# Kernel tuning notes

Measured on AMD Instinct MI355X. Metric: run time of the kernel, lower is better.

## Reference

```python
import jax, jax.numpy as jnp
import numpy as np

TOPK = 20
EPS = 1e-5
NEG_SLOPE = 0.2


def _bn(x, gamma, beta):
    # BatchNorm1d in training mode: stats over all but the channel (last) axis.
    axes = tuple(range(x.ndim - 1))
    m = x.mean(axes, keepdims=True)
    v = x.var(axes, keepdims=True)  # biased variance, as torch uses for normalization
    return (x - m) * jax.lax.rsqrt(v + EPS) * gamma + beta


def setup_inputs() -> dict:
    key = jax.random.key(0)
    ks = jax.random.split(key, 12)
    B, N, F, D, K = 64, 512, 64, 64, TOPK
    H = 32  # slide_win // 2
    return {
        "data": jax.random.normal(ks[0], (B, N, F), jnp.float32),
        "org_edge_index": jax.random.randint(ks[1], (2, 10), 0, N),  # unused by forward math
        "emb_table": jax.random.normal(ks[2], (N, D), jnp.float32) * 0.1,
        "W_gnn": jax.random.normal(ks[3], (D, F), jnp.float32) / jnp.sqrt(F),
        "att_i": jax.random.normal(ks[4], (D,), jnp.float32) / jnp.sqrt(D),
        "att_j": jax.random.normal(ks[5], (D,), jnp.float32) / jnp.sqrt(D),
        "att_em_i": jax.random.normal(ks[6], (D,), jnp.float32) / jnp.sqrt(D),
        "att_em_j": jax.random.normal(ks[7], (D,), jnp.float32) / jnp.sqrt(D),
        "bias_gnn": jnp.zeros((D,), jnp.float32),
        "bn1_g": jnp.ones((D,), jnp.float32), "bn1_b": jnp.zeros((D,), jnp.float32),
        "bn2_g": jnp.ones((D,), jnp.float32), "bn2_b": jnp.zeros((D,), jnp.float32),
        "lin_W": jax.random.normal(ks[8], (H, D), jnp.float32) / jnp.sqrt(D),
        "lin_b": jnp.zeros((H,), jnp.float32),
        "out_W": jax.random.normal(ks[9], (2 * H, H), jnp.float32) / jnp.sqrt(H),
        "out_b": jnp.zeros((2 * H,), jnp.float32),
    }


def reference(data, org_edge_index, emb_table, W_gnn, att_i, att_j, att_em_i, att_em_j,
              bias_gnn, bn1_g, bn1_b, bn2_g, bn2_b, lin_W, lin_b, out_W, out_b):
    B, N, F = data.shape
    # --- top-k cosine-similarity graph (embeddings are detached in the original) ---
    w = emb_table  # (N, D)
    nrm = jnp.linalg.norm(w, axis=-1)
    cos = (w @ w.T) / (nrm[:, None] * nrm[None, :])
    _, topk_idx = jax.lax.top_k(cos, TOPK)  # (N, K); col 0 is the self loop (cos=1)
    # Every target node i has exactly TOPK incoming edges j in topk_idx[i];
    # remove_self_loops + add_self_loops is set-equivalent to this edge set.

    # --- GraphLayer (GAT-style, heads=1, concat=False) ---
    xw = jnp.einsum('bnf,df->bnd', data, W_gnn)  # (B, N, D)
    a_i = xw @ att_i + w @ att_em_i              # (B, N), per-target scalar
    a_j = xw @ att_j + w @ att_em_j              # (B, N), per-source scalar
    alpha = a_i[:, :, None] + a_j[:, topk_idx]   # (B, N, K): gather sources per target
    alpha = jax.nn.leaky_relu(alpha, NEG_SLOPE)
    alpha = jax.nn.softmax(alpha, axis=-1)       # segment softmax over fixed-size neighborhoods
    xj = xw[:, topk_idx]                         # (B, N, K, D) edge gather (memory-bound)
    out = jnp.einsum('bnk,bnkd->bnd', alpha, xj) + bias_gnn  # scatter-aggregate

    # GNNLayer: BatchNorm1d over (B*N) rows + ReLU
    out = jax.nn.relu(_bn(out, bn1_g, bn1_b))

    # --- head ---
    out = out * w                                 # x * embedding(idx)
    out = jax.nn.relu(_bn(out, bn2_g, bn2_b))     # bn_outlayer_in over (B, D, N)
    out = out @ lin_W.T + lin_b                   # (B, N, slide_win//2)
    out = out @ out_W.T + out_b                   # OutLayer, single Linear -> (B, N, slide_win)
    return out
```

## Files before the change

### kernel.cpp

```cpp
#include <hip/hip_runtime.h>
#include <math.h>

#define Bb 64
#define Nn 512
#define Ff 64
#define Dd 64
#define Kk 20
#define Hh 32
#define ROWS (Bb*Nn)
#define EPSc 1e-5f
#define NEG 0.2f


__device__ __forceinline__ float dot4(float4 a, float4 b) {
    return a.x*b.x + a.y*b.y + a.z*b.z + a.w*b.w;
}
__device__ __forceinline__ void xr4(float4& a, int m) {
    a.x += __shfl_xor(a.x, m); a.y += __shfl_xor(a.y, m);
    a.z += __shfl_xor(a.z, m); a.w += __shfl_xor(a.w, m);
}

__global__ __launch_bounds__(256) void k_p1(const float* __restrict__ data,
                                            const float* __restrict__ emb,
                                            const float* __restrict__ Wg,
                                            const float* __restrict__ att_i,
                                            const float* __restrict__ att_j,
                                            const float* __restrict__ att_em_i,
                                            const float* __restrict__ att_em_j,
                                            int* __restrict__ topk,
                                            float* __restrict__ ai,
                                            float* __restrict__ aj,
                                            float* __restrict__ xw) {
    __shared__ __align__(16) float shbuf[576];
    int t = threadIdx.x, blk = blockIdx.x;
    if (blk < Nn) {
        float* wish = shbuf;
        float* sv   = shbuf + 64;
        int i = blk;
        if (t < 64) {
            float wv = emb[i*64 + t];
            float ss = wv*wv;
            #pragma unroll
            for (int s = 32; s > 0; s >>= 1) ss += __shfl_xor(ss, s);
            wish[t] = wv * (1.f / sqrtf(ss));
        }
        __syncthreads();
        int seg = t & 3, jl = t >> 2;
        const float4* wish4 = (const float4*)wish;
        float4 wn[4];
        #pragma unroll
        for (int q = 0; q < 4; q++) wn[q] = wish4[seg*4 + q];
        const float4* emb4 = (const float4*)emb;
        for (int jb = 0; jb < 8; jb++) {
            int j = jb*64 + jl;
            float p = 0.f, s2 = 0.f;
            #pragma unroll
            for (int q = 0; q < 4; q++) {
                float4 e = emb4[j*16 + seg*4 + q];
                p += dot4(e, wn[q]); s2 += dot4(e, e);
            }
            p  += __shfl_xor(p, 1);  p  += __shfl_xor(p, 2);
            s2 += __shfl_xor(s2, 1); s2 += __shfl_xor(s2, 2);
            if (seg == 0) sv[j] = p * (1.f / sqrtf(s2));
        }
        __syncthreads();
        if (t < 64) {
            float v[8];
            #pragma unroll
            for (int q = 0; q < 8; q++) v[q] = sv[q*64 + t];
            for (int k = 0; k < Kk; k++) {
                float bv = v[0]; int bi = t;
                #pragma unroll
                for (int q = 1; q < 8; q++)
                    if (v[q] > bv) { bv = v[q]; bi = q*64 + t; }
                #pragma unroll
                for (int s = 1; s < 64; s <<= 1) {
                    float ov = __shfl_xor(bv, s); int oi = __shfl_xor(bi, s);
                    if (ov > bv || (ov == bv && oi < bi)) { bv = ov; bi = oi; }
                }
                if (t == 0) topk[i*Kk + k] = bi;
                #pragma unroll
                for (int q = 0; q < 8; q++)
                    if (bi == q*64 + t) v[q] = -INFINITY;
            }
        }
    } else {
        float* sh = shbuf;
        int d = t & 63, r = t >> 6;
        const float4* wg4 = (const float4*)Wg;
        float4 w4[16];
        #pragma unroll
        for (int q = 0; q < 16; q++) w4[q] = wg4[d*16 + q];
        float atti = att_i[d], attj = att_j[d];
        float aemi = att_em_i[d], aemj = att_em_j[d];
        const float4* sh4 = (const float4*)sh;
        for (int it = 0; it < 16; it++) {
            int g = (blk - Nn)*16 + it;
            sh[t] = data[g*256 + t];
            float acc = 0.f;
            #pragma unroll
            for (int q = 0; q < 16; q++) acc += dot4(sh4[r*16 + q], w4[q]);
            int row = g*4 + r;
            xw[row*64 + d] = acc;
            int n = row & (Nn - 1);
            float wv = emb[n*64 + d];
            float vi = acc*atti + wv*aemi;
            float vj = acc*attj + wv*aemj;
            #pragma unroll
            for (int s = 32; s > 0; s >>= 1) { vi += __shfl_xor(vi, s); vj += __shfl_xor(vj, s); }
            if (d == 0) { ai[row] = vi; aj[row] = vj; }
        }
    }
}

__global__ __launch_bounds__(256) void k_alpha(const float* __restrict__ ai,
                                               const float* __restrict__ aj,
                                               const int* __restrict__ topk,
                                               float* __restrict__ alpha) {
    int t = threadIdx.x;
    int hw = t >> 5, k = t & 31;
    int row = blockIdx.x*8 + hw;
    int b = row >> 9, n = row & (Nn - 1);
    int base = b << 9;
    float aival = ai[row];
    float v = -1e30f;
    if (k < Kk) {
        int j = topk[n*Kk + k];
        float x = aival + aj[base + j];
        v = x > 0.f ? x : NEG * x;
    }
    float m = v;
    #pragma unroll
    for (int s = 1; s <= 16; s <<= 1) m = fmaxf(m, __shfl_xor(m, s));
    float e = (k < Kk) ? __expf(v - m) : 0.f;
    float es = e;
    #pragma unroll
    for (int s = 1; s <= 16; s <<= 1) es += __shfl_xor(es, s);
    if (k < Kk) alpha[row*Kk + k] = e / es;
}

__global__ __launch_bounds__(256) void k_pv(const float* __restrict__ xw,
                                            const float* __restrict__ alpha,
                                            const int* __restrict__ topk,
                                            const float* __restrict__ bias,
                                            float* __restrict__ gout,
                                            float* __restrict__ part1) {
    __shared__ float ssum[4][64], ssq[4][64];
    int t = threadIdx.x;
    int d = t & 63, r = t >> 6;
    const int4*   topk4  = (const int4*)topk;
    const float4* alpha4 = (const float4*)alpha;
    float bias_d = bias[d];
    float lsum = 0.f, lsq = 0.f;
    #pragma unroll 4
    for (int it = 0; it < 16; it++) {
        int row = blockIdx.x*64 + it*4 + r;
        int n = row & (Nn - 1);
        int base = row & ~(Nn - 1);
        float acc = bias_d;
        #pragma unroll
        for (int c = 0; c < 5; c++) {
            int4   jj = topk4[n*5 + c];
            float4 aa = alpha4[row*5 + c];
            acc += aa.x * xw[(base + jj.x)*64 + d];
            acc += aa.y * xw[(base + jj.y)*64 + d];
            acc += aa.z * xw[(base + jj.z)*64 + d];
            acc += aa.w * xw[(base + jj.w)*64 + d];
        }
        gout[row*64 + d] = acc;
        lsum += acc; lsq += acc*acc;
    }
    ssum[r][d] = lsum; ssq[r][d] = lsq;
    __syncthreads();
    if (t < 64) {
        float s1 = ssum[0][t] + ssum[1][t] + ssum[2][t] + ssum[3][t];
        float s2 = ssq[0][t] + ssq[1][t] + ssq[2][t] + ssq[3][t];
        part1[blockIdx.x*128 + t]      = s1;
        part1[blockIdx.x*128 + 64 + t] = s2;
    }
}

__global__ __launch_bounds__(1024) void k_red(const float* __restrict__ part, int nb,
                                              const float* __restrict__ g,
                                              const float* __restrict__ bta,
                                              float* __restrict__ AC) {
    __shared__ float sh1[16][64], sh2[16][64];
    int t = threadIdx.x, d = t & 63, qt = t >> 6;
    float s1 = 0.f, s2 = 0.f;
    for (int b = qt; b < nb; b += 16) {
        s1 += part[b*128 + d];
        s2 += part[b*128 + 64 + d];
    }
    sh1[qt][d] = s1; sh2[qt][d] = s2;
    __syncthreads();
    if (t < 64) {
        float t1 = 0.f, t2 = 0.f;
        #pragma unroll
        for (int i = 0; i < 16; i++) { t1 += sh1[i][t]; t2 += sh2[i][t]; }
        float mean = t1 * (1.f/ROWS);
        float var  = t2 * (1.f/ROWS) - mean*mean;
        float A = (1.f / sqrtf(var + EPSc)) * g[t];
        AC[t]      = A;
        AC[64 + t] = bta[t] - mean * A;
    }
}

__global__ __launch_bounds__(256) void k_bn1(float* __restrict__ gout,
                                             const float* __restrict__ emb,
                                             const float* __restrict__ AC1,
                                             float* __restrict__ part2) {
    __shared__ __align__(16) float4 s1[4][16], s2[4][16];
    int t = threadIdx.x, q = t & 15;
    float4 A4 = ((const float4*)AC1)[q];
    float4 C4 = ((const float4*)AC1)[16 + q];
    float4 sum4 = {0,0,0,0}, sq4 = {0,0,0,0};
    #pragma unroll
    for (int i = 0; i < 4; i++) {
        int f = blockIdx.x*1024 + i*256 + t;
        int row = f >> 4, n = row & (Nn - 1);
        float4 x = ((float4*)gout)[f];
        float4 wv = ((const float4*)emb)[n*16 + q];
        float4 v;
        v.x = fmaxf(x.x*A4.x + C4.x, 0.f) * wv.x;
        v.y = fmaxf(x.y*A4.y + C4.y, 0.f) * wv.y;
        v.z = fmaxf(x.z*A4.z + C4.z, 0.f) * wv.z;
        v.w = fmaxf(x.w*A4.w + C4.w, 0.f) * wv.w;
        ((float4*)gout)[f] = v;
        sum4.x += v.x; sum4.y += v.y; sum4.z += v.z; sum4.w += v.w;
        sq4.x += v.x*v.x; sq4.y += v.y*v.y; sq4.z += v.z*v.z; sq4.w += v.w*v.w;
    }
    xr4(sum4, 16); xr4(sum4, 32);
    xr4(sq4, 16);  xr4(sq4, 32);
    int l = t & 63, w = t >> 6;
    if (l < 16) { s1[w][q] = sum4; s2[w][q] = sq4; }
    __syncthreads();
    if (t < 16) {
        float4 a = s1[0][t], c = s2[0][t];
        #pragma unroll
        for (int ww = 1; ww < 4; ww++) {
            float4 x1 = s1[ww][t], x2 = s2[ww][t];
            a.x += x1.x; a.y += x1.y; a.z += x1.z; a.w += x1.w;
            c.x += x2.x; c.y += x2.y; c.z += x2.z; c.w += x2.w;
        }
        ((float4*)part2)[blockIdx.x*32 + t]      = a;
        ((float4*)part2)[blockIdx.x*32 + 16 + t] = c;
    }
}

__global__ __launch_bounds__(256) void k_head2(const float* __restrict__ y,
                                               const float* __restrict__ AC2,
                                               const float* __restrict__ linW,
                                               const float* __restrict__ linb,
                                               const float* __restrict__ outW,
                                               const float* __restrict__ outb,
                                               float* __restrict__ out) {
    __shared__ __align__(16) float zsh[4][64];
    __shared__ __align__(16) float hsh[4][32];
    int t = threadIdx.x;
    int d = t & 63, r = t >> 6;
    int j = d & 31, half = d >> 5;
    float A = AC2[d], C = AC2[64 + d];
    const float4* linW4 = (const float4*)linW;
    const float4* outW4 = (const float4*)outW;
    float4 lw4[8], ow4[8];
    #pragma unroll
    for (int q = 0; q < 8; q++) lw4[q] = linW4[j*16 + half*8 + q];
    #pragma unroll
    for (int q = 0; q < 8; q++) ow4[q] = outW4[d*8 + q];
    float lb = linb[j], ob = outb[d];
    const float4* zsh4 = (const float4*)zsh;
    const float4* hsh4 = (const float4*)hsh;
    for (int it = 0; it < 16; it++) {
        int row = blockIdx.x*64 + it*4 + r;
        float x = y[row*64 + d];
        float z = fmaxf(x*A + C, 0.f);
        zsh[r][d] = z;
        float p = 0.f;
        #pragma unroll
        for (int q = 0; q < 8; q++) p += dot4(zsh4[r*16 + half*8 + q], lw4[q]);
        p += __shfl_xor(p, 32);
        if (half == 0) hsh[r][j] = p + lb;
        float o = ob;
        #pragma unroll
        for (int q = 0; q < 8; q++) o += dot4(hsh4[r*8 + q], ow4[q]);
        out[row*64 + d] = o;
    }
}

extern "C" void kernel_launch(void* const* d_in, const int* in_sizes, int n_in,
                              void* d_out, int out_size, void* d_ws, size_t ws_size,
                              hipStream_t stream) {
    const float* data     = (const float*)d_in[0];
    const float* emb      = (const float*)d_in[2];
    const float* Wg       = (const float*)d_in[3];
    const float* att_i    = (const float*)d_in[4];
    const float* att_j    = (const float*)d_in[5];
    const float* att_em_i = (const float*)d_in[6];
    const float* att_em_j = (const float*)d_in[7];
    const float* bias     = (const float*)d_in[8];
    const float* bn1_g    = (const float*)d_in[9];
    const float* bn1_b    = (const float*)d_in[10];
    const float* bn2_g    = (const float*)d_in[11];
    const float* bn2_b    = (const float*)d_in[12];
    const float* linW     = (const float*)d_in[13];
    const float* linb     = (const float*)d_in[14];
    const float* outW     = (const float*)d_in[15];
    const float* outb     = (const float*)d_in[16];
    float* out = (float*)d_out;

    float* ws    = (float*)d_ws;
    int*   topk  = (int*)(ws + 512);
    float* AC1   = ws + 10752;
    float* AC2   = ws + 10880;
    float* a_i   = ws + 11264;
    float* a_j   = ws + 44032;
    float* xw    = ws + 76800;
    float* gout  = ws + 2173952;
    float* alpha = out;
    float* part1 = out + 786432;
    float* part2 = out + 1048576;

    k_p1   <<<1024, 256, 0, stream>>>(data, emb, Wg, att_i, att_j, att_em_i, att_em_j,
                                      topk, a_i, a_j, xw);
    k_alpha<<<ROWS/8, 256, 0, stream>>>(a_i, a_j, topk, alpha);
    k_pv   <<<512, 256, 0, stream>>>(xw, alpha, topk, bias, gout, part1);
    k_red  <<<1, 1024, 0, stream>>>(part1, 512, bn1_g, bn1_b, AC1);
    k_bn1  <<<512, 256, 0, stream>>>(gout, emb, AC1, part2);
    k_red  <<<1, 1024, 0, stream>>>(part2, 512, bn2_g, bn2_b, AC2);
    k_head2<<<512, 256, 0, stream>>>(gout, AC2, linW, linb, outW, outb, out);
}
```

Before: 187.8 us.

## Fuse all stages into one persistent kernel with hierarchical grid barriers

Replaces the seven separate launches with a single 512-block persistent kernel. Stages are separated by a custom two-level atomic grid barrier, and the last-arriving block does each BatchNorm reduction. Softmax alpha weights now stay in LDS instead of going through global memory. This removes launch gaps and the single-block reduction kernels. In exchange it relies on all 512 blocks being co-resident, adds a memset, and adds spin-wait costs.

```diff
diff --git a/kernel.cpp b/kernel.cpp
--- a/kernel.cpp
+++ b/kernel.cpp
@@ -1,15 +1,14 @@
 #include <hip/hip_runtime.h>
 #include <math.h>
 
-#define Bb 64
 #define Nn 512
 #define Ff 64
 #define Dd 64
 #define Kk 20
-#define Hh 32
-#define ROWS (Bb*Nn)
+#define ROWS 32768
 #define EPSc 1e-5f
 #define NEG 0.2f
+#define NB 512
 
 
 __device__ __forceinline__ float dot4(float4 a, float4 b) {
@@ -20,33 +19,77 @@
     a.z += __shfl_xor(a.z, m); a.w += __shfl_xor(a.w, m);
 }
 
-__global__ __launch_bounds__(256) void k_p1(const float* __restrict__ data,
-                                            const float* __restrict__ emb,
-                                            const float* __restrict__ Wg,
-                                            const float* __restrict__ att_i,
-                                            const float* __restrict__ att_j,
-                                            const float* __restrict__ att_em_i,
-                                            const float* __restrict__ att_em_j,
-                                            int* __restrict__ topk,
-                                            float* __restrict__ ai,
-                                            float* __restrict__ aj,
-                                            float* __restrict__ xw) {
-    __shared__ __align__(16) float shbuf[576];
+union SMem {
+    struct { float wish[64]; float sv[512]; } p1a;
+    struct { float sh[256]; } p1b;
+    struct { float a_lds[64][20]; float ssum[4][64]; float ssq[4][64]; } p23;
+    struct { float red[2][128]; } pr;
+    struct { float4 s1[4][16]; float4 s2[4][16]; } p5;
+    struct { float zsh[4][64]; float hsh[4][32]; } p7;
+};
+
+__device__ __forceinline__ int gbar_arrive(int* ctr, int phase) {
+    __shared__ int s_role;
+    int t = threadIdx.x, g = blockIdx.x >> 6;
+    __syncthreads();
+    if (t == 0) {
+        __threadfence();
+        int a = atomicAdd(&ctr[g*32], 1);
+        int r = 0;
+        if (a == 64*phase - 1) {
+            int b = atomicAdd(&ctr[256], 1);
+            r = (b == 8*phase - 1) ? 2 : 1;
+        }
+        s_role = r;
+    }
+    __syncthreads();
+    return s_role;
+}
+__device__ __forceinline__ void gbar_wait(int* ctr, int phase, int role) {
+    int t = threadIdx.x, g = blockIdx.x >> 6;
+    if (t == 0) {
+        if (role == 2) { __threadfence(); atomicExch(&ctr[544], phase); }
+        if (role >= 1) {
+            while (atomicAdd(&ctr[544], 0) < phase) __builtin_amdgcn_s_sleep(2);
+            atomicExch(&ctr[288 + g*32], phase);
+        } else {
+            while (atomicAdd(&ctr[288 + g*32], 0) < phase) __builtin_amdgcn_s_sleep(2);
+        }
+    }
+    __syncthreads();
+}
+
+__global__ __launch_bounds__(256, 2) void k_fused(
+        const float* __restrict__ data, const float* __restrict__ emb,
+        const float* __restrict__ Wg,
+        const float* __restrict__ att_i, const float* __restrict__ att_j,
+        const float* __restrict__ att_em_i, const float* __restrict__ att_em_j,
+        const float* __restrict__ bias,
+        const float* __restrict__ bn1_g, const float* __restrict__ bn1_b,
+        const float* __restrict__ bn2_g, const float* __restrict__ bn2_b,
+        const float* __restrict__ linW, const float* __restrict__ linb,
+        const float* __restrict__ outW, const float* __restrict__ outb,
+        float* __restrict__ out,
+        int* __restrict__ topk, float* __restrict__ ai, float* __restrict__ aj,
+        float* __restrict__ xw, float* __restrict__ gout,
+        float* __restrict__ AC1, float* __restrict__ AC2,
+        float* __restrict__ part1, float* __restrict__ part2,
+        int* __restrict__ ctr) {
+    __shared__ __align__(16) SMem sm;
     int t = threadIdx.x, blk = blockIdx.x;
-    if (blk < Nn) {
-        float* wish = shbuf;
-        float* sv   = shbuf + 64;
+
+    {
         int i = blk;
         if (t < 64) {
             float wv = emb[i*64 + t];
             float ss = wv*wv;
             #pragma unroll
             for (int s = 32; s > 0; s >>= 1) ss += __shfl_xor(ss, s);
-            wish[t] = wv * (1.f / sqrtf(ss));
+            sm.p1a.wish[t] = wv * (1.f / sqrtf(ss));
         }
         __syncthreads();
         int seg = t & 3, jl = t >> 2;
-        const float4* wish4 = (const float4*)wish;
+        const float4* wish4 = (const float4*)sm.p1a.wish;
         float4 wn[4];
         #pragma unroll
         for (int q = 0; q < 4; q++) wn[q] = wish4[seg*4 + q];
@@ -61,13 +104,13 @@
             }
             p  += __shfl_xor(p, 1);  p  += __shfl_xor(p, 2);
             s2 += __shfl_xor(s2, 1); s2 += __shfl_xor(s2, 2);
-            if (seg == 0) sv[j] = p * (1.f / sqrtf(s2));
+            if (seg == 0) sm.p1a.sv[j] = p * (1.f / sqrtf(s2));
         }
         __syncthreads();
         if (t < 64) {
             float v[8];
             #pragma unroll
-            for (int q = 0; q < 8; q++) v[q] = sv[q*64 + t];
+            for (int q = 0; q < 8; q++) v[q] = sm.p1a.sv[q*64 + t];
             for (int k = 0; k < Kk; k++) {
                 float bv = v[0]; int bi = t;
                 #pragma unroll
@@ -84,8 +127,11 @@
                     if (bi == q*64 + t) v[q] = -INFINITY;
             }
         }
-    } else {
-        float* sh = shbuf;
+    }
+    __syncthreads();
+
+    {
+        float* sh = sm.p1b.sh;
         int d = t & 63, r = t >> 6;
         const float4* wg4 = (const float4*)Wg;
         float4 w4[16];
@@ -95,12 +141,12 @@
         float aemi = att_em_i[d], aemj = att_em_j[d];
         const float4* sh4 = (const float4*)sh;
         for (int it = 0; it < 16; it++) {
-            int g = (blk - Nn)*16 + it;
-            sh[t] = data[g*256 + t];
+            int g2 = blk*16 + it;
+            sh[t] = data[g2*256 + t];
             float acc = 0.f;
             #pragma unroll
             for (int q = 0; q < 16; q++) acc += dot4(sh4[r*16 + q], w4[q]);
-            int row = g*4 + r;
+            int row = g2*4 + r;
             xw[row*64 + d] = acc;
             int n = row & (Nn - 1);
             float wv = emb[n*64 + d];
@@ -111,179 +157,180 @@
             if (d == 0) { ai[row] = vi; aj[row] = vj; }
         }
     }
-}
-
-__global__ __launch_bounds__(256) void k_alpha(const float* __restrict__ ai,
-                                               const float* __restrict__ aj,
-                                               const int* __restrict__ topk,
-                                               float* __restrict__ alpha) {
-    int t = threadIdx.x;
-    int hw = t >> 5, k = t & 31;
-    int row = blockIdx.x*8 + hw;
-    int b = row >> 9, n = row & (Nn - 1);
-    int base = b << 9;
-    float aival = ai[row];
-    float v = -1e30f;
-    if (k < Kk) {
-        int j = topk[n*Kk + k];
-        float x = aival + aj[base + j];
-        v = x > 0.f ? x : NEG * x;
-    }
-    float m = v;
-    #pragma unroll
-    for (int s = 1; s <= 16; s <<= 1) m = fmaxf(m, __shfl_xor(m, s));
-    float e = (k < Kk) ? __expf(v - m) : 0.f;
-    float es = e;
-    #pragma unroll
-    for (int s = 1; s <= 16; s <<= 1) es += __shfl_xor(es, s);
-    if (k < Kk) alpha[row*Kk + k] = e / es;
-}
-
-__global__ __launch_bounds__(256) void k_pv(const float* __restrict__ xw,
-                                            const float* __restrict__ alpha,
-                                            const int* __restrict__ topk,
-                                            const float* __restrict__ bias,
-                                            float* __restrict__ gout,
-                                            float* __restrict__ part1) {
-    __shared__ float ssum[4][64], ssq[4][64];
-    int t = threadIdx.x;
-    int d = t & 63, r = t >> 6;
-    const int4*   topk4  = (const int4*)topk;
-    const float4* alpha4 = (const float4*)alpha;
-    float bias_d = bias[d];
-    float lsum = 0.f, lsq = 0.f;
-    #pragma unroll 4
-    for (int it = 0; it < 16; it++) {
-        int row = blockIdx.x*64 + it*4 + r;
-        int n = row & (Nn - 1);
-        int base = row & ~(Nn - 1);
-        float acc = bias_d;
-        #pragma unroll
-        for (int c = 0; c < 5; c++) {
-            int4   jj = topk4[n*5 + c];
-            float4 aa = alpha4[row*5 + c];
-            acc += aa.x * xw[(base + jj.x)*64 + d];
-            acc += aa.y * xw[(base + jj.y)*64 + d];
-            acc += aa.z * xw[(base + jj.z)*64 + d];
-            acc += aa.w * xw[(base + jj.w)*64 + d];
-        }
-        gout[row*64 + d] = acc;
-        lsum += acc; lsq += acc*acc;
-    }
-    ssum[r][d] = lsum; ssq[r][d] = lsq;
-    __syncthreads();
-    if (t < 64) {
-        float s1 = ssum[0][t] + ssum[1][t] + ssum[2][t] + ssum[3][t];
-        float s2 = ssq[0][t] + ssq[1][t] + ssq[2][t] + ssq[3][t];
-        part1[blockIdx.x*128 + t]      = s1;
-        part1[blockIdx.x*128 + 64 + t] = s2;
-    }
-}
-
-__global__ __launch_bounds__(1024) void k_red(const float* __restrict__ part, int nb,
-                                              const float* __restrict__ g,
-                                              const float* __restrict__ bta,
-                                              float* __restrict__ AC) {
-    __shared__ float sh1[16][64], sh2[16][64];
-    int t = threadIdx.x, d = t & 63, qt = t >> 6;
-    float s1 = 0.f, s2 = 0.f;
-    for (int b = qt; b < nb; b += 16) {
-        s1 += part[b*128 + d];
-        s2 += part[b*128 + 64 + d];
-    }
-    sh1[qt][d] = s1; sh2[qt][d] = s2;
-    __syncthreads();
-    if (t < 64) {
-        float t1 = 0.f, t2 = 0.f;
-        #pragma unroll
-        for (int i = 0; i < 16; i++) { t1 += sh1[i][t]; t2 += sh2[i][t]; }
-        float mean = t1 * (1.f/ROWS);
-        float var  = t2 * (1.f/ROWS) - mean*mean;
-        float A = (1.f / sqrtf(var + EPSc)) * g[t];
-        AC[t]      = A;
-        AC[64 + t] = bta[t] - mean * A;
-    }
-}
-
-__global__ __launch_bounds__(256) void k_bn1(float* __restrict__ gout,
-                                             const float* __restrict__ emb,
-                                             const float* __restrict__ AC1,
-                                             float* __restrict__ part2) {
-    __shared__ __align__(16) float4 s1[4][16], s2[4][16];
-    int t = threadIdx.x, q = t & 15;
-    float4 A4 = ((const float4*)AC1)[q];
-    float4 C4 = ((const float4*)AC1)[16 + q];
-    float4 sum4 = {0,0,0,0}, sq4 = {0,0,0,0};
-    #pragma unroll
-    for (int i = 0; i < 4; i++) {
-        int f = blockIdx.x*1024 + i*256 + t;
-        int row = f >> 4, n = row & (Nn - 1);
-        float4 x = ((float4*)gout)[f];
-        float4 wv = ((const float4*)emb)[n*16 + q];
-        float4 v;
-        v.x = fmaxf(x.x*A4.x + C4.x, 0.f) * wv.x;
-        v.y = fmaxf(x.y*A4.y + C4.y, 0.f) * wv.y;
-        v.z = fmaxf(x.z*A4.z + C4.z, 0.f) * wv.z;
-        v.w = fmaxf(x.w*A4.w + C4.w, 0.f) * wv.w;
-        ((float4*)gout)[f] = v;
-        sum4.x += v.x; sum4.y += v.y; sum4.z += v.z; sum4.w += v.w;
-        sq4.x += v.x*v.x; sq4.y += v.y*v.y; sq4.z += v.z*v.z; sq4.w += v.w*v.w;
-    }
-    xr4(sum4, 16); xr4(sum4, 32);
-    xr4(sq4, 16);  xr4(sq4, 32);
-    int l = t & 63, w = t >> 6;
-    if (l < 16) { s1[w][q] = sum4; s2[w][q] = sq4; }
-    __syncthreads();
-    if (t < 16) {
-        float4 a = s1[0][t], c = s2[0][t];
-        #pragma unroll
-        for (int ww = 1; ww < 4; ww++) {
-            float4 x1 = s1[ww][t], x2 = s2[ww][t];
-            a.x += x1.x; a.y += x1.y; a.z += x1.z; a.w += x1.w;
-            c.x += x2.x; c.y += x2.y; c.z += x2.z; c.w += x2.w;
-        }
-        ((float4*)part2)[blockIdx.x*32 + t]      = a;
-        ((float4*)part2)[blockIdx.x*32 + 16 + t] = c;
-    }
-}
-
-__global__ __launch_bounds__(256) void k_head2(const float* __restrict__ y,
-                                               const float* __restrict__ AC2,
-                                               const float* __restrict__ linW,
-                                               const float* __restrict__ linb,
-                                               const float* __restrict__ outW,
-                                               const float* __restrict__ outb,
-                                               float* __restrict__ out) {
-    __shared__ __align__(16) float zsh[4][64];
-    __shared__ __align__(16) float hsh[4][32];
-    int t = threadIdx.x;
-    int d = t & 63, r = t >> 6;
-    int j = d & 31, half = d >> 5;
-    float A = AC2[d], C = AC2[64 + d];
-    const float4* linW4 = (const float4*)linW;
-    const float4* outW4 = (const float4*)outW;
-    float4 lw4[8], ow4[8];
-    #pragma unroll
-    for (int q = 0; q < 8; q++) lw4[q] = linW4[j*16 + half*8 + q];
-    #pragma unroll
-    for (int q = 0; q < 8; q++) ow4[q] = outW4[d*8 + q];
-    float lb = linb[j], ob = outb[d];
-    const float4* zsh4 = (const float4*)zsh;
-    const float4* hsh4 = (const float4*)hsh;
-    for (int it = 0; it < 16; it++) {
-        int row = blockIdx.x*64 + it*4 + r;
-        float x = y[row*64 + d];
-        float z = fmaxf(x*A + C, 0.f);
-        zsh[r][d] = z;
-        float p = 0.f;
-        #pragma unroll
-        for (int q = 0; q < 8; q++) p += dot4(zsh4[r*16 + half*8 + q], lw4[q]);
-        p += __shfl_xor(p, 32);
-        if (half == 0) hsh[r][j] = p + lb;
-        float o = ob;
-        #pragma unroll
-        for (int q = 0; q < 8; q++) o += dot4(hsh4[r*8 + q], ow4[q]);
-        out[row*64 + d] = o;
+
+    { int role = gbar_arrive(ctr, 1); gbar_wait(ctr, 1, role); }
+
+    {
+        int hw = t >> 5, k = t & 31;
+        for (int it = 0; it < 8; it++) {
+            int lr = it*8 + hw;
+            int row = blk*64 + lr;
+            int b = row >> 9, n = row & (Nn - 1);
+            int base = b << 9;
+            float aival = ai[row];
+            float v = -1e30f; int j = 0;
+            if (k < Kk) {
+                j = topk[n*Kk + k];
+                float x = aival + aj[base + j];
+                v = x > 0.f ? x : NEG * x;
+            }
+            float m = v;
+            #pragma unroll
+            for (int s = 1; s <= 16; s <<= 1) m = fmaxf(m, __shfl_xor(m, s));
+            float e = (k < Kk) ? __expf(v - m) : 0.f;
+            float es = e;
+            #pragma unroll
+            for (int s = 1; s <= 16; s <<= 1) es += __shfl_xor(es, s);
+            if (k < Kk) sm.p23.a_lds[lr][k] = e / es;
+        }
+    }
+    __syncthreads();
+
+    {
+        int d = t & 63, r = t >> 6;
+        const int4* topk4 = (const int4*)topk;
+        const float4* a4 = (const float4*)&sm.p23.a_lds[0][0];
+        float bias_d = bias[d];
+        float lsum = 0.f, lsq = 0.f;
+        #pragma unroll 4
+        for (int it = 0; it < 16; it++) {
+            int lr = it*4 + r;
+            int row = blk*64 + lr;
+            int n = row & (Nn - 1);
+            int base = row & ~(Nn - 1);
+            float acc = bias_d;
+            #pragma unroll
+            for (int c = 0; c < 5; c++) {
+                int4   jj = topk4[n*5 + c];
+                float4 aa = a4[lr*5 + c];
+                acc += aa.x * xw[(base + jj.x)*64 + d];
+                acc += aa.y * xw[(base + jj.y)*64 + d];
+                acc += aa.z * xw[(base + jj.z)*64 + d];
+                acc += aa.w * xw[(base + jj.w)*64 + d];
+            }
+            gout[row*64 + d] = acc;
+            lsum += acc; lsq += acc*acc;
+        }
+        sm.p23.ssum[r][d] = lsum; sm.p23.ssq[r][d] = lsq;
+        __syncthreads();
+        if (t < 64) {
+            float s1 = sm.p23.ssum[0][t] + sm.p23.ssum[1][t] + sm.p23.ssum[2][t] + sm.p23.ssum[3][t];
+            float s2 = sm.p23.ssq[0][t]  + sm.p23.ssq[1][t]  + sm.p23.ssq[2][t]  + sm.p23.ssq[3][t];
+            part1[blk*128 + t]      = s1;
+            part1[blk*128 + 64 + t] = s2;
+        }
+    }
+
+    {
+        int role = gbar_arrive(ctr, 2);
+        if (role == 2) {
+            int ch = t & 127, half = t >> 7;
+            float s = 0.f;
+            for (int b2 = half; b2 < NB; b2 += 2) s += part1[b2*128 + ch];
+            sm.pr.red[half][ch] = s;
+            __syncthreads();
+            if (t < 64) {
+                float ts = sm.pr.red[0][t]      + sm.pr.red[1][t];
+                float tq = sm.pr.red[0][64 + t] + sm.pr.red[1][64 + t];
+                float mean = ts * (1.f/ROWS);
+                float var  = tq * (1.f/ROWS) - mean*mean;
+                float A = (1.f / sqrtf(var + EPSc)) * bn1_g[t];
+                AC1[t] = A; AC1[64 + t] = bn1_b[t] - mean * A;
+            }
+            __syncthreads();
+        }
+        gbar_wait(ctr, 2, role);
+    }
+
+    {
+        int q = t & 15;
+        float4 A4 = ((const float4*)AC1)[q];
+        float4 C4 = ((const float4*)AC1)[16 + q];
+        float4 sum4 = {0,0,0,0}, sq4 = {0,0,0,0};
+        #pragma unroll
+        for (int i = 0; i < 4; i++) {
+            int f = blk*1024 + i*256 + t;
+            int row = f >> 4, n = row & (Nn - 1);
+            float4 x = ((float4*)gout)[f];
+            float4 wv = ((const float4*)emb)[n*16 + q];
+            float4 v;
+            v.x = fmaxf(x.x*A4.x + C4.x, 0.f) * wv.x;
+            v.y = fmaxf(x.y*A4.y + C4.y, 0.f) * wv.y;
+            v.z = fmaxf(x.z*A4.z + C4.z, 0.f) * wv.z;
+            v.w = fmaxf(x.w*A4.w + C4.w, 0.f) * wv.w;
+            ((float4*)gout)[f] = v;
+            sum4.x += v.x; sum4.y += v.y; sum4.z += v.z; sum4.w += v.w;
+            sq4.x += v.x*v.x; sq4.y += v.y*v.y; sq4.z += v.z*v.z; sq4.w += v.w*v.w;
+        }
+        xr4(sum4, 16); xr4(sum4, 32);
+        xr4(sq4, 16);  xr4(sq4, 32);
+        int l = t & 63, w = t >> 6;
+        __syncthreads();
+        if (l < 16) { sm.p5.s1[w][q] = sum4; sm.p5.s2[w][q] = sq4; }
+        __syncthreads();
+        if (t < 16) {
+            float4 a = sm.p5.s1[0][t], c = sm.p5.s2[0][t];
+            #pragma unroll
+            for (int ww = 1; ww < 4; ww++) {
+                float4 x1 = sm.p5.s1[ww][t], x2 = sm.p5.s2[ww][t];
+                a.x += x1.x; a.y += x1.y; a.z += x1.z; a.w += x1.w;
+                c.x += x2.x; c.y += x2.y; c.z += x2.z; c.w += x2.w;
+            }
+            ((float4*)part2)[blk*32 + t]      = a;
+            ((float4*)part2)[blk*32 + 16 + t] = c;
+        }
+    }
+
+    {
+        int role = gbar_arrive(ctr, 3);
+        if (role == 2) {
+            int ch = t & 127, half = t >> 7;
+            float s = 0.f;
+            for (int b2 = half; b2 < NB; b2 += 2) s += part2[b2*128 + ch];
+            sm.pr.red[half][ch] = s;
+            __syncthreads();
+            if (t < 64) {
+                float ts = sm.pr.red[0][t]      + sm.pr.red[1][t];
+                float tq = sm.pr.red[0][64 + t] + sm.pr.red[1][64 + t];
+                float mean = ts * (1.f/ROWS);
+                float var  = tq * (1.f/ROWS) - mean*mean;
+                float A = (1.f / sqrtf(var + EPSc)) * bn2_g[t];
+                AC2[t] = A; AC2[64 + t] = bn2_b[t] - mean * A;
+            }
+            __syncthreads();
+        }
+        gbar_wait(ctr, 3, role);
+    }
+
+    {
+        int d = t & 63, r = t >> 6;
+        int j = d & 31, half = d >> 5;
+        float A = AC2[d], C = AC2[64 + d];
+        const float4* linW4 = (const float4*)linW;
+        const float4* outW4 = (const float4*)outW;
+        float4 lw4[8], ow4[8];
+        #pragma unroll
+        for (int q = 0; q < 8; q++) lw4[q] = linW4[j*16 + half*8 + q];
+        #pragma unroll
+        for (int q = 0; q < 8; q++) ow4[q] = outW4[d*8 + q];
+        float lb = linb[j], ob = outb[d];
+        const float4* zsh4 = (const float4*)sm.p7.zsh;
+        const float4* hsh4 = (const float4*)sm.p7.hsh;
+        for (int it = 0; it < 16; it++) {
+            int row = blk*64 + it*4 + r;
+            float x = gout[row*64 + d];
+            float z = fmaxf(x*A + C, 0.f);
+            sm.p7.zsh[r][d] = z;
+            float p = 0.f;
+            #pragma unroll
+            for (int q = 0; q < 8; q++) p += dot4(zsh4[r*16 + half*8 + q], lw4[q]);
+            p += __shfl_xor(p, 32);
+            if (half == 0) sm.p7.hsh[r][j] = p + lb;
+            float o = ob;
+            #pragma unroll
+            for (int q = 0; q < 8; q++) o += dot4(hsh4[r*8 + q], ow4[q]);
+            out[row*64 + d] = o;
+        }
     }
 }
 
@@ -316,16 +363,14 @@
     float* a_j   = ws + 44032;
     float* xw    = ws + 76800;
     float* gout  = ws + 2173952;
-    float* alpha = out;
-    float* part1 = out + 786432;
-    float* part2 = out + 1048576;
-
-    k_p1   <<<1024, 256, 0, stream>>>(data, emb, Wg, att_i, att_j, att_em_i, att_em_j,
-                                      topk, a_i, a_j, xw);
-    k_alpha<<<ROWS/8, 256, 0, stream>>>(a_i, a_j, topk, alpha);
-    k_pv   <<<512, 256, 0, stream>>>(xw, alpha, topk, bias, gout, part1);
-    k_red  <<<1, 1024, 0, stream>>>(part1, 512, bn1_g, bn1_b, AC1);
-    k_bn1  <<<512, 256, 0, stream>>>(gout, emb, AC1, part2);
-    k_red  <<<1, 1024, 0, stream>>>(part2, 512, bn2_g, bn2_b, AC2);
-    k_head2<<<512, 256, 0, stream>>>(gout, AC2, linW, linb, outW, outb, out);
-}
+    int*   ctr   = (int*)(ws + 4271104);
+    float* part1 = ws + 4271744;
+    float* part2 = ws + 4337280;
+
+    hipMemsetAsync(ctr, 0, 576 * sizeof(int), stream);
+    k_fused<<<NB, 256, 0, stream>>>(data, emb, Wg, att_i, att_j, att_em_i, att_em_j,
+                                    bias, bn1_g, bn1_b, bn2_g, bn2_b,
+                                    linW, linb, outW, outb, out,
+                                    topk, a_i, a_j, xw, gout,
+                                    AC1, AC2, part1, part2, ctr);
+}
```

Result: slower. 381.0 us (+102.9%).

## Fuse softmax into aggregation and fold BN reductions into last-block tails

Applied to the files above, without the earlier changes.

Computes the attention softmax inside the aggregation kernel and keeps alpha in shared memory instead of writing it to global memory and reading it back. Replaces the two single-block BatchNorm reduction kernels with a last-block-done pattern: an atomic counter picks the final block, which reduces the per-block partial sums and writes the scale/shift coefficients. This removes three kernel launches and the alpha round trip, at the cost of a memset, atomics and thread fences, and a serial tail run by one block.

```diff
diff --git a/kernel.cpp b/kernel.cpp
--- a/kernel.cpp
+++ b/kernel.cpp
@@ -1,15 +1,14 @@
 #include <hip/hip_runtime.h>
 #include <math.h>
 
-#define Bb 64
 #define Nn 512
 #define Ff 64
 #define Dd 64
 #define Kk 20
-#define Hh 32
-#define ROWS (Bb*Nn)
+#define ROWS 32768
 #define EPSc 1e-5f
 #define NEG 0.2f
+#define NB 512
 
 
 __device__ __forceinline__ float dot4(float4 a, float4 b) {
@@ -18,6 +17,58 @@
 __device__ __forceinline__ void xr4(float4& a, int m) {
     a.x += __shfl_xor(a.x, m); a.y += __shfl_xor(a.y, m);
     a.z += __shfl_xor(a.z, m); a.w += __shfl_xor(a.w, m);
+}
+
+union SMemPV {
+    struct { float a_lds[64][20]; float ssum[4][64]; float ssq[4][64]; } p;
+    struct { float4 red[8][32]; } pr;
+};
+union SMemBN {
+    struct { float4 s1[4][16]; float4 s2[4][16]; } p;
+    struct { float4 red[8][32]; } pr;
+};
+
+template <typename SM>
+__device__ __forceinline__ void tail_reduce(const float* __restrict__ part,
+                                            const float* __restrict__ g,
+                                            const float* __restrict__ bta,
+                                            float* __restrict__ AC, SM& sm) {
+    int t = threadIdx.x;
+    int ch4 = t & 31, h = t >> 5;
+    const float4* p4 = (const float4*)part;
+    float4 s = {0,0,0,0};
+    for (int b = h; b < NB; b += 8) {
+        float4 v = p4[b*32 + ch4];
+        s.x += v.x; s.y += v.y; s.z += v.z; s.w += v.w;
+    }
+    sm.pr.red[h][ch4] = s;
+    __syncthreads();
+    if (t < 32) {
+        float4 a = sm.pr.red[0][t];
+        #pragma unroll
+        for (int i = 1; i < 8; i++) {
+            float4 v = sm.pr.red[i][t];
+            a.x += v.x; a.y += v.y; a.z += v.z; a.w += v.w;
+        }
+        sm.pr.red[0][t] = a;
+    }
+    __syncthreads();
+    if (t < 16) {
+        float4 s4 = sm.pr.red[0][t], q4 = sm.pr.red[0][16 + t];
+        float4 A4, C4;
+        const float* sp = &s4.x; const float* qp = &q4.x;
+        float* Ap = &A4.x; float* Cp = &C4.x;
+        #pragma unroll
+        for (int c = 0; c < 4; c++) {
+            int d = 4*t + c;
+            float mean = sp[c] * (1.f/ROWS);
+            float var  = qp[c] * (1.f/ROWS) - mean*mean;
+            float A = (1.f / sqrtf(var + EPSc)) * g[d];
+            Ap[c] = A; Cp[c] = bta[d] - mean * A;
+        }
+        ((float4*)AC)[t]      = A4;
+        ((float4*)AC)[16 + t] = C4;
+    }
 }
 
 __global__ __launch_bounds__(256) void k_p1(const float* __restrict__ data,
@@ -113,110 +164,110 @@
     }
 }
 
-__global__ __launch_bounds__(256) void k_alpha(const float* __restrict__ ai,
-                                               const float* __restrict__ aj,
-                                               const int* __restrict__ topk,
-                                               float* __restrict__ alpha) {
-    int t = threadIdx.x;
-    int hw = t >> 5, k = t & 31;
-    int row = blockIdx.x*8 + hw;
-    int b = row >> 9, n = row & (Nn - 1);
-    int base = b << 9;
-    float aival = ai[row];
-    float v = -1e30f;
-    if (k < Kk) {
-        int j = topk[n*Kk + k];
-        float x = aival + aj[base + j];
-        v = x > 0.f ? x : NEG * x;
-    }
-    float m = v;
-    #pragma unroll
-    for (int s = 1; s <= 16; s <<= 1) m = fmaxf(m, __shfl_xor(m, s));
-    float e = (k < Kk) ? __expf(v - m) : 0.f;
-    float es = e;
-    #pragma unroll
-    for (int s = 1; s <= 16; s <<= 1) es += __shfl_xor(es, s);
-    if (k < Kk) alpha[row*Kk + k] = e / es;
-}
-
-__global__ __launch_bounds__(256) void k_pv(const float* __restrict__ xw,
-                                            const float* __restrict__ alpha,
-                                            const int* __restrict__ topk,
-                                            const float* __restrict__ bias,
-                                            float* __restrict__ gout,
-                                            float* __restrict__ part1) {
-    __shared__ float ssum[4][64], ssq[4][64];
-    int t = threadIdx.x;
-    int d = t & 63, r = t >> 6;
-    const int4*   topk4  = (const int4*)topk;
-    const float4* alpha4 = (const float4*)alpha;
-    float bias_d = bias[d];
-    float lsum = 0.f, lsq = 0.f;
-    #pragma unroll 4
-    for (int it = 0; it < 16; it++) {
-        int row = blockIdx.x*64 + it*4 + r;
-        int n = row & (Nn - 1);
-        int base = row & ~(Nn - 1);
-        float acc = bias_d;
-        #pragma unroll
-        for (int c = 0; c < 5; c++) {
-            int4   jj = topk4[n*5 + c];
-            float4 aa = alpha4[row*5 + c];
-            acc += aa.x * xw[(base + jj.x)*64 + d];
-            acc += aa.y * xw[(base + jj.y)*64 + d];
-            acc += aa.z * xw[(base + jj.z)*64 + d];
-            acc += aa.w * xw[(base + jj.w)*64 + d];
-        }
-        gout[row*64 + d] = acc;
-        lsum += acc; lsq += acc*acc;
-    }
-    ssum[r][d] = lsum; ssq[r][d] = lsq;
-    __syncthreads();
-    if (t < 64) {
-        float s1 = ssum[0][t] + ssum[1][t] + ssum[2][t] + ssum[3][t];
-        float s2 = ssq[0][t] + ssq[1][t] + ssq[2][t] + ssq[3][t];
-        part1[blockIdx.x*128 + t]      = s1;
-        part1[blockIdx.x*128 + 64 + t] = s2;
-    }
-}
-
-__global__ __launch_bounds__(1024) void k_red(const float* __restrict__ part, int nb,
-                                              const float* __restrict__ g,
-                                              const float* __restrict__ bta,
-                                              float* __restrict__ AC) {
-    __shared__ float sh1[16][64], sh2[16][64];
-    int t = threadIdx.x, d = t & 63, qt = t >> 6;
-    float s1 = 0.f, s2 = 0.f;
-    for (int b = qt; b < nb; b += 16) {
-        s1 += part[b*128 + d];
-        s2 += part[b*128 + 64 + d];
-    }
-    sh1[qt][d] = s1; sh2[qt][d] = s2;
-    __syncthreads();
-    if (t < 64) {
-        float t1 = 0.f, t2 = 0.f;
-        #pragma unroll
-        for (int i = 0; i < 16; i++) { t1 += sh1[i][t]; t2 += sh2[i][t]; }
-        float mean = t1 * (1.f/ROWS);
-        float var  = t2 * (1.f/ROWS) - mean*mean;
-        float A = (1.f / sqrtf(var + EPSc)) * g[t];
-        AC[t]      = A;
-        AC[64 + t] = bta[t] - mean * A;
-    }
-}
-
-__global__ __launch_bounds__(256) void k_bn1(float* __restrict__ gout,
+__global__ __launch_bounds__(256) void k_pv2(const float* __restrict__ xw,
+                                             const float* __restrict__ ai,
+                                             const float* __restrict__ aj,
+                                             const int* __restrict__ topk,
+                                             const float* __restrict__ bias,
+                                             const float* __restrict__ bn1_g,
+                                             const float* __restrict__ bn1_b,
+                                             float* __restrict__ gout,
+                                             float* __restrict__ part1,
+                                             float* __restrict__ AC1,
+                                             int* __restrict__ ctr) {
+    __shared__ __align__(16) SMemPV sm;
+    __shared__ int s_last;
+    int t = threadIdx.x, blk = blockIdx.x;
+
+    {
+        int hw = t >> 5, k = t & 31;
+        for (int it = 0; it < 8; it++) {
+            int lr = it*8 + hw;
+            int row = blk*64 + lr;
+            int n = row & (Nn - 1);
+            int base = row & ~(Nn - 1);
+            float aival = ai[row];
+            float v = -1e30f;
+            if (k < Kk) {
+                int j = topk[n*Kk + k];
+                float x = aival + aj[base + j];
+                v = x > 0.f ? x : NEG * x;
+            }
+            float m = v;
+            #pragma unroll
+            for (int s = 1; s <= 16; s <<= 1) m = fmaxf(m, __shfl_xor(m, s));
+            float e = (k < Kk) ? __expf(v - m) : 0.f;
+            float es = e;
+            #pragma unroll
+            for (int s = 1; s <= 16; s <<= 1) es += __shfl_xor(es, s);
+            if (k < Kk) sm.p.a_lds[lr][k] = e / es;
+        }
+    }
+    __syncthreads();
+
+    {
+        int d = t & 63, r = t >> 6;
+        const int4* topk4 = (const int4*)topk;
+        const float4* a4 = (const float4*)&sm.p.a_lds[0][0];
+        float bias_d = bias[d];
+        float lsum = 0.f, lsq = 0.f;
+        #pragma unroll 4
+        for (int it = 0; it < 16; it++) {
+            int lr = it*4 + r;
+            int row = blk*64 + lr;
+            int n = row & (Nn - 1);
+            int base = row & ~(Nn - 1);
+            float acc = bias_d;
+            #pragma unroll
+            for (int c = 0; c < 5; c++) {
+                int4   jj = topk4[n*5 + c];
+                float4 aa = a4[lr*5 + c];
+                acc += aa.x * xw[(base + jj.x)*64 + d];
+                acc += aa.y * xw[(base + jj.y)*64 + d];
+                acc += aa.z * xw[(base + jj.z)*64 + d];
+                acc += aa.w * xw[(base + jj.w)*64 + d];
+            }
+            gout[row*64 + d] = acc;
+            lsum += acc; lsq += acc*acc;
+        }
+        sm.p.ssum[r][d] = lsum; sm.p.ssq[r][d] = lsq;
+        __syncthreads();
+        if (t < 64) {
+            float s1 = sm.p.ssum[0][t] + sm.p.ssum[1][t] + sm.p.ssum[2][t] + sm.p.ssum[3][t];
+            float s2 = sm.p.ssq[0][t]  + sm.p.ssq[1][t]  + sm.p.ssq[2][t]  + sm.p.ssq[3][t];
+            part1[blk*128 + t]      = s1;
+            part1[blk*128 + 64 + t] = s2;
+        }
+    }
+    __syncthreads();
+    if (t == 0) {
+        __threadfence();
+        s_last = (atomicAdd(ctr, 1) == NB - 1);
+    }
+    __syncthreads();
+    if (s_last) {
+        __threadfence();
+        tail_reduce(part1, bn1_g, bn1_b, AC1, sm);
+    }
+}
+
+__global__ __launch_bounds__(256) void k_bn2(float* __restrict__ gout,
                                              const float* __restrict__ emb,
                                              const float* __restrict__ AC1,
-                                             float* __restrict__ part2) {
-    __shared__ __align__(16) float4 s1[4][16], s2[4][16];
-    int t = threadIdx.x, q = t & 15;
+                                             const float* __restrict__ bn2_g,
+                                             const float* __restrict__ bn2_b,
+                                             float* __restrict__ part2,
+                                             float* __restrict__ AC2,
+                                             int* __restrict__ ctr) {
+    __shared__ __align__(16) SMemBN sm;
+    __shared__ int s_last;
+    int t = threadIdx.x, blk = blockIdx.x, q = t & 15;
     float4 A4 = ((const float4*)AC1)[q];
     float4 C4 = ((const float4*)AC1)[16 + q];
     float4 sum4 = {0,0,0,0}, sq4 = {0,0,0,0};
     #pragma unroll
     for (int i = 0; i < 4; i++) {
-        int f = blockIdx.x*1024 + i*256 + t;
+        int f = blk*1024 + i*256 + t;
         int row = f >> 4, n = row & (Nn - 1);
         float4 x = ((float4*)gout)[f];
         float4 wv = ((const float4*)emb)[n*16 + q];
@@ -232,22 +283,32 @@
     xr4(sum4, 16); xr4(sum4, 32);
     xr4(sq4, 16);  xr4(sq4, 32);
     int l = t & 63, w = t >> 6;
-    if (l < 16) { s1[w][q] = sum4; s2[w][q] = sq4; }
+    if (l < 16) { sm.p.s1[w][q] = sum4; sm.p.s2[w][q] = sq4; }
     __syncthreads();
     if (t < 16) {
-        float4 a = s1[0][t], c = s2[0][t];
+        float4 a = sm.p.s1[0][t], c = sm.p.s2[0][t];
         #pragma unroll
         for (int ww = 1; ww < 4; ww++) {
-            float4 x1 = s1[ww][t], x2 = s2[ww][t];
+            float4 x1 = sm.p.s1[ww][t], x2 = sm.p.s2[ww][t];
             a.x += x1.x; a.y += x1.y; a.z += x1.z; a.w += x1.w;
             c.x += x2.x; c.y += x2.y; c.z += x2.z; c.w += x2.w;
         }
-        ((float4*)part2)[blockIdx.x*32 + t]      = a;
-        ((float4*)part2)[blockIdx.x*32 + 16 + t] = c;
-    }
-}
-
-__global__ __launch_bounds__(256) void k_head2(const float* __restrict__ y,
+        ((float4*)part2)[blk*32 + t]      = a;
+        ((float4*)part2)[blk*32 + 16 + t] = c;
+    }
+    __syncthreads();
+    if (t == 0) {
+        __threadfence();
+        s_last = (atomicAdd(ctr, 1) == NB - 1);
+    }
+    __syncthreads();
+    if (s_last) {
+        __threadfence();
+        tail_reduce(part2, bn2_g, bn2_b, AC2, sm);
+    }
+}
+
+__global__ __launch_bounds__(256) void k_head3(const float* __restrict__ y,
                                                const float* __restrict__ AC2,
                                                const float* __restrict__ linW,
                                                const float* __restrict__ linb,
@@ -316,16 +377,16 @@
     float* a_j   = ws + 44032;
     float* xw    = ws + 76800;
     float* gout  = ws + 2173952;
-    float* alpha = out;
-    float* part1 = out + 786432;
-    float* part2 = out + 1048576;
-
+    int*   ctr   = (int*)(ws + 4271104);
+    float* part1 = ws + 4271744;
+    float* part2 = ws + 4337280;
+
+    hipMemsetAsync(ctr, 0, 64 * sizeof(int), stream);
     k_p1   <<<1024, 256, 0, stream>>>(data, emb, Wg, att_i, att_j, att_em_i, att_em_j,
                                       topk, a_i, a_j, xw);
-    k_alpha<<<ROWS/8, 256, 0, stream>>>(a_i, a_j, topk, alpha);
-    k_pv   <<<512, 256, 0, stream>>>(xw, alpha, topk, bias, gout, part1);
-    k_red  <<<1, 1024, 0, stream>>>(part1, 512, bn1_g, bn1_b, AC1);
-    k_bn1  <<<512, 256, 0, stream>>>(gout, emb, AC1, part2);
-    k_red  <<<1, 1024, 0, stream>>>(part2, 512, bn2_g, bn2_b, AC2);
-    k_head2<<<512, 256, 0, stream>>>(gout, AC2, linW, linb, outW, outb, out);
-}
+    k_pv2  <<<NB, 256, 0, stream>>>(xw, a_i, a_j, topk, bias, bn1_g, bn1_b,
+                                    gout, part1, AC1, ctr);
+    k_bn2  <<<NB, 256, 0, stream>>>(gout, emb, AC1, bn2_g, bn2_b,
+                                    part2, AC2, ctr + 32);
+    k_head3<<<NB, 256, 0, stream>>>(gout, AC2, linW, linb, outW, outb, out);
+}
```

Measured after the change: 233.5 us. 1.24x slower.

## Fuse attention softmax into aggregation kernel and remap blocks for XCD locality

Applied to the files above, without the earlier changes.

Removes the separate alpha kernel: each aggregation block now computes the leaky-relu softmax weights for its 32 rows into shared memory, then gathers neighbour features. This drops the alpha round-trip through global memory and one launch. Blocks in both the projection and aggregation kernels are remapped so that each XCD handles a contiguous set of batches, meant to keep the gathered xw rows in that XCD's L2. The aggregation grid doubles to 1024 blocks, so the BN1 partial-sum reduction now covers 1024 partials, and the partial buffers move from the output buffer to the workspace.

```diff
diff --git a/kernel.cpp b/kernel.cpp
--- a/kernel.cpp
+++ b/kernel.cpp
@@ -1,13 +1,11 @@
 #include <hip/hip_runtime.h>
 #include <math.h>
 
-#define Bb 64
 #define Nn 512
 #define Ff 64
 #define Dd 64
 #define Kk 20
-#define Hh 32
-#define ROWS (Bb*Nn)
+#define ROWS 32768
 #define EPSc 1e-5f
 #define NEG 0.2f
 
@@ -18,6 +16,14 @@
 __device__ __forceinline__ void xr4(float4& a, int m) {
     a.x += __shfl_xor(a.x, m); a.y += __shfl_xor(a.y, m);
     a.z += __shfl_xor(a.z, m); a.w += __shfl_xor(a.w, m);
+}
+__device__ __forceinline__ int xcd_row0_64(int bb) {
+    int xcd = bb & 7, i = bb >> 3;
+    return (xcd*8 + (i & 7))*512 + (i >> 3)*64;
+}
+__device__ __forceinline__ int xcd_row0_32(int bb) {
+    int xcd = bb & 7, i = bb >> 3;
+    return (xcd*8 + (i & 7))*512 + (i >> 3)*32;
 }
 
 __global__ __launch_bounds__(256) void k_p1(const float* __restrict__ data,
@@ -94,8 +100,9 @@
         float atti = att_i[d], attj = att_j[d];
         float aemi = att_em_i[d], aemj = att_em_j[d];
         const float4* sh4 = (const float4*)sh;
+        int row0 = xcd_row0_64(blk - Nn);
         for (int it = 0; it < 16; it++) {
-            int g = (blk - Nn)*16 + it;
+            int g = (row0 >> 2) + it;
             sh[t] = data[g*256 + t];
             float acc = 0.f;
             #pragma unroll
@@ -113,70 +120,78 @@
     }
 }
 
-__global__ __launch_bounds__(256) void k_alpha(const float* __restrict__ ai,
-                                               const float* __restrict__ aj,
-                                               const int* __restrict__ topk,
-                                               float* __restrict__ alpha) {
-    int t = threadIdx.x;
-    int hw = t >> 5, k = t & 31;
-    int row = blockIdx.x*8 + hw;
-    int b = row >> 9, n = row & (Nn - 1);
-    int base = b << 9;
-    float aival = ai[row];
-    float v = -1e30f;
-    if (k < Kk) {
-        int j = topk[n*Kk + k];
-        float x = aival + aj[base + j];
-        v = x > 0.f ? x : NEG * x;
-    }
-    float m = v;
-    #pragma unroll
-    for (int s = 1; s <= 16; s <<= 1) m = fmaxf(m, __shfl_xor(m, s));
-    float e = (k < Kk) ? __expf(v - m) : 0.f;
-    float es = e;
-    #pragma unroll
-    for (int s = 1; s <= 16; s <<= 1) es += __shfl_xor(es, s);
-    if (k < Kk) alpha[row*Kk + k] = e / es;
-}
-
 __global__ __launch_bounds__(256) void k_pv(const float* __restrict__ xw,
-                                            const float* __restrict__ alpha,
+                                            const float* __restrict__ ai,
+                                            const float* __restrict__ aj,
                                             const int* __restrict__ topk,
                                             const float* __restrict__ bias,
                                             float* __restrict__ gout,
                                             float* __restrict__ part1) {
+    __shared__ __align__(16) float a_lds[32][20];
     __shared__ float ssum[4][64], ssq[4][64];
-    int t = threadIdx.x;
-    int d = t & 63, r = t >> 6;
-    const int4*   topk4  = (const int4*)topk;
-    const float4* alpha4 = (const float4*)alpha;
-    float bias_d = bias[d];
-    float lsum = 0.f, lsq = 0.f;
-    #pragma unroll 4
-    for (int it = 0; it < 16; it++) {
-        int row = blockIdx.x*64 + it*4 + r;
-        int n = row & (Nn - 1);
-        int base = row & ~(Nn - 1);
-        float acc = bias_d;
-        #pragma unroll
-        for (int c = 0; c < 5; c++) {
-            int4   jj = topk4[n*5 + c];
-            float4 aa = alpha4[row*5 + c];
-            acc += aa.x * xw[(base + jj.x)*64 + d];
-            acc += aa.y * xw[(base + jj.y)*64 + d];
-            acc += aa.z * xw[(base + jj.z)*64 + d];
-            acc += aa.w * xw[(base + jj.w)*64 + d];
-        }
-        gout[row*64 + d] = acc;
-        lsum += acc; lsq += acc*acc;
-    }
-    ssum[r][d] = lsum; ssq[r][d] = lsq;
+    int t = threadIdx.x, blk = blockIdx.x;
+    int row0 = xcd_row0_32(blk);
+
+    {
+        int hw = t >> 5, k = t & 31;
+        #pragma unroll
+        for (int it = 0; it < 4; it++) {
+            int lr = it*8 + hw;
+            int row = row0 + lr;
+            int n = row & (Nn - 1);
+            int base = row & ~(Nn - 1);
+            float aival = ai[row];
+            float v = -1e30f;
+            if (k < Kk) {
+                int j = topk[n*Kk + k];
+                float x = aival + aj[base + j];
+                v = x > 0.f ? x : NEG * x;
+            }
+            float m = v;
+            #pragma unroll
+            for (int s = 1; s <= 16; s <<= 1) m = fmaxf(m, __shfl_xor(m, s));
+            float e = (k < Kk) ? __expf(v - m) : 0.f;
+            float es = e;
+            #pragma unroll
+            for (int s = 1; s <= 16; s <<= 1) es += __shfl_xor(es, s);
+            if (k < Kk) a_lds[lr][k] = e / es;
+        }
+    }
     __syncthreads();
-    if (t < 64) {
-        float s1 = ssum[0][t] + ssum[1][t] + ssum[2][t] + ssum[3][t];
-        float s2 = ssq[0][t] + ssq[1][t] + ssq[2][t] + ssq[3][t];
-        part1[blockIdx.x*128 + t]      = s1;
-        part1[blockIdx.x*128 + 64 + t] = s2;
+
+    {
+        int d = t & 63, r = t >> 6;
+        const int4* topk4 = (const int4*)topk;
+        const float4* a4 = (const float4*)&a_lds[0][0];
+        float bias_d = bias[d];
+        float lsum = 0.f, lsq = 0.f;
+        #pragma unroll 4
+        for (int it = 0; it < 8; it++) {
+            int lr = it*4 + r;
+            int row = row0 + lr;
+            int n = row & (Nn - 1);
+            int base = row & ~(Nn - 1);
+            float acc = bias_d;
+            #pragma unroll
+            for (int c = 0; c < 5; c++) {
+                int4   jj = topk4[n*5 + c];
+                float4 aa = a4[lr*5 + c];
+                acc += aa.x * xw[(base + jj.x)*64 + d];
+                acc += aa.y * xw[(base + jj.y)*64 + d];
+                acc += aa.z * xw[(base + jj.z)*64 + d];
+                acc += aa.w * xw[(base + jj.w)*64 + d];
+            }
+            gout[row*64 + d] = acc;
+            lsum += acc; lsq += acc*acc;
+        }
+        ssum[r][d] = lsum; ssq[r][d] = lsq;
+        __syncthreads();
+        if (t < 64) {
+            float s1 = ssum[0][t] + ssum[1][t] + ssum[2][t] + ssum[3][t];
+            float s2 = ssq[0][t] + ssq[1][t] + ssq[2][t] + ssq[3][t];
+            part1[blk*128 + t]      = s1;
+            part1[blk*128 + 64 + t] = s2;
+        }
     }
 }
 
@@ -247,7 +262,7 @@
     }
 }
 
-__global__ __launch_bounds__(256) void k_head2(const float* __restrict__ y,
+__global__ __launch_bounds__(256) void k_head3(const float* __restrict__ y,
                                                const float* __restrict__ AC2,
                                                const float* __restrict__ linW,
                                                const float* __restrict__ linb,
@@ -316,16 +331,14 @@
     float* a_j   = ws + 44032;
     float* xw    = ws + 76800;
     float* gout  = ws + 2173952;
-    float* alpha = out;
-    float* part1 = out + 786432;
-    float* part2 = out + 1048576;
+    float* part1 = ws + 4271744;
+    float* part2 = ws + 4402816;
 
     k_p1   <<<1024, 256, 0, stream>>>(data, emb, Wg, att_i, att_j, att_em_i, att_em_j,
                                       topk, a_i, a_j, xw);
-    k_alpha<<<ROWS/8, 256, 0, stream>>>(a_i, a_j, topk, alpha);
-    k_pv   <<<512, 256, 0, stream>>>(xw, alpha, topk, bias, gout, part1);
-    k_red  <<<1, 1024, 0, stream>>>(part1, 512, bn1_g, bn1_b, AC1);
+    k_pv   <<<1024, 256, 0, stream>>>(xw, a_i, a_j, topk, bias, gout, part1);
+    k_red  <<<1, 1024, 0, stream>>>(part1, 1024, bn1_g, bn1_b, AC1);
     k_bn1  <<<512, 256, 0, stream>>>(gout, emb, AC1, part2);
     k_red  <<<1, 1024, 0, stream>>>(part2, 512, bn2_g, bn2_b, AC2);
-    k_head2<<<512, 256, 0, stream>>>(gout, AC2, linW, linb, outW, outb, out);
-}
+    k_head3<<<512, 256, 0, stream>>>(gout, AC2, linW, linb, outW, outb, out);
+}
```

Result: no change. 184.4 us (-1.8%).
